# Kernel tuning notes

Hardware: AMD Instinct MI355X
Metric: run time of the kernel (lower is better)

## Reference

```python
import jax, jax.numpy as jnp
import numpy as np

RADIUS = 9.0
GROUPS = 4
BLK = 64  # row block for streaming the N x N pairwise convolution


def leaky(x):
    return jnp.where(x >= 0, x, 0.2 * x)


def group_norm(x, gamma, beta, eps=1e-5):
    # x: (N, C); matches torch.nn.GroupNorm(GROUPS, C) applied to (1, C, N)
    N, C = x.shape
    xg = x.T.reshape(GROUPS, (C // GROUPS) * N)
    m = xg.mean(axis=1, keepdims=True)
    v = ((xg - m) ** 2).mean(axis=1, keepdims=True)
    xg = (xg - m) / jnp.sqrt(v + eps)
    return xg.reshape(C, N).T * gamma + beta


def tangent_vectors(n):
    # Duff et al. orthonormal tangent basis; n: (N,3) unit normals -> (N,2,3)
    x, y, z = n[:, 0], n[:, 1], n[:, 2]
    s = jnp.where(z >= 0, 1.0, -1.0)
    a = -1.0 / (s + z)
    b = x * y * a
    uv = jnp.stack([1 + s * x * x * a, s * b, -s * x, b, s + y * y * a, -y], axis=-1)
    return uv.reshape(-1, 2, 3)


def load_mesh(xyz, normals, weights):
    # Build oriented local frames nuv (N,3,3) as in dMaSIFConv_seg.load_mesh
    p = xyz / RADIUS
    uv = tangent_vectors(normals)                  # (N,2,3)
    diff = p[None, :, :] - p[:, None, :]           # (N,N,3): x_j - x_i
    d2 = jnp.sum(diff * diff, axis=-1)             # (N,N)
    cos = normals @ normals.T                      # (N,N)
    window = jnp.exp(-d2 * (2.0 - cos) ** 2)       # pseudo-geodesic Gaussian
    X = jnp.einsum('ikd,ijd->ijk', uv, diff)       # (N,N,2) tangent coords
    ov = jnp.einsum('ij,j,ijk->ik', window, weights[:, 0], X) + 1e-5  # (N,2)
    nrm = jnp.maximum(jnp.linalg.norm(ov, axis=-1, keepdims=True), 1e-12)
    ov = ov / nrm                                  # F.normalize
    ex, ey = ov[:, :1], ov[:, 1:]
    u, v = uv[:, 0, :], uv[:, 1, :]
    return jnp.stack([normals, ex * u + ey * v, -ey * u + ex * v], axis=1)


def dmasif_conv(points, nuv, feats,
                ni_w1, ni_b1, ni_w2, ni_b2, gn_in_g, gn_in_b,
                cv_a1, cv_b1, cv_a2, cv_b2,
                no_w1, no_b1, no_w2, no_b2, gn_out_g, gn_out_b):
    N = points.shape[0]
    H = ni_w1.shape[0]
    O = no_w1.shape[0]
    # net_in + GroupNorm
    h = leaky(feats @ ni_w1.T + ni_b1)
    h = leaky(h @ ni_w2.T + ni_b2)
    h = group_norm(h, gn_in_g, gn_in_b)            # (N,H)
    p = points / (np.sqrt(2.0) * RADIUS)
    n = jax.lax.stop_gradient(nuv[:, 0, :])        # normals detached in window

    p_blk = p.reshape(-1, BLK, 3)
    n_blk = n.reshape(-1, BLK, 3)
    nuv_blk = nuv.reshape(-1, BLK, 3, 3)

    @jax.checkpoint
    def step(carry, blk):
        pi, ni, nuvi = blk                                  # (B,3),(B,3),(B,3,3)
        diff = p[None, :, :] - pi[:, None, :]               # (B,N,3)
        d2 = jnp.sum(diff * diff, axis=-1)                  # (B,N)
        window = jnp.exp(-d2 * (2.0 - ni @ n.T) ** 2)       # (B,N)
        X = jnp.einsum('bkd,bnd->bnk', nuvi, diff)          # (B,N,3) local coords
        g = jax.nn.relu(jnp.einsum('bnk,ck->bnc', X, cv_a1) + cv_b1)  # (B,N,8)
        M = jax.nn.relu(jnp.einsum('bnc,fc->bnf', g, cv_a2) + cv_b2)  # (B,N,H*O)
        M = M.reshape(BLK, N, O, H)
        out = jnp.einsum('bn,bnoh,nh->bo', window, M, h)    # (B,O)
        return carry, out

    _, outs = jax.lax.scan(step, None, (p_blk, n_blk, nuv_blk))
    y = outs.reshape(N, O)
    y = leaky(y @ no_w1.T + no_b1)
    y = leaky(y @ no_w2.T + no_b2)
    return group_norm(y, gn_out_g, gn_out_b)


def setup_inputs() -> dict:
    key = jax.random.key(0)
    ks = jax.random.split(key, 32)
    N, I, U, H, O, C = 4096, 16, 16, 16, 16, 8
    nrm = jax.random.normal(ks[1], (N, 3), dtype=jnp.float32)
    nrm = nrm / jnp.linalg.norm(nrm, axis=-1, keepdims=True)
    w = lambda k, sh: 0.1 * jax.random.normal(k, sh, dtype=jnp.float32)
    return {
        'surface_xyz': 10.0 * jax.random.normal(ks[0], (N, 3), dtype=jnp.float32),
        'surface_normals': nrm,
        'features': jax.random.normal(ks[2], (N, I), dtype=jnp.float32),
        'os_w1': w(ks[3], (U, I)), 'os_b1': w(ks[4], (U,)),
        'os_w2': w(ks[5], (1, U)), 'os_b2': w(ks[6], (1,)),
        'ni_w1': w(ks[7], (H, I)), 'ni_b1': w(ks[8], (H,)),
        'ni_w2': w(ks[9], (H, H)), 'ni_b2': w(ks[10], (H,)),
        'gn_in_g': jnp.ones((H,), jnp.float32), 'gn_in_b': jnp.zeros((H,), jnp.float32),
        'cv_a1': w(ks[11], (C, 3)), 'cv_b1': w(ks[12], (C,)),
        'cv_a2': w(ks[13], (H * O, C)), 'cv_b2': w(ks[14], (H * O,)),
        'no_w1': w(ks[15], (O, H)), 'no_b1': w(ks[16], (O,)),
        'no_w2': w(ks[17], (O, O)), 'no_b2': w(ks[18], (O,)),
        'gn_out_g': jnp.ones((O,), jnp.float32), 'gn_out_b': jnp.zeros((O,), jnp.float32),
        'll_w1': w(ks[19], (O, O)), 'll_b1': w(ks[20], (O,)),
        'll_w2': w(ks[21], (O, O)), 'll_b2': w(ks[22], (O,)),
        'lt_w': w(ks[23], (O, I)), 'lt_b': w(ks[24], (O,)),
    }


def reference(surface_xyz, surface_normals, features,
              os_w1, os_b1, os_w2, os_b2,
              ni_w1, ni_b1, ni_w2, ni_b2, gn_in_g, gn_in_b,
              cv_a1, cv_b1, cv_a2, cv_b2,
              no_w1, no_b1, no_w2, no_b2, gn_out_g, gn_out_b,
              ll_w1, ll_b1, ll_w2, ll_b2, lt_w, lt_b):
    # orientation scores: Linear -> LeakyReLU(0.2) -> Linear
    scores = leaky(features @ os_w1.T + os_b1) @ os_w2.T + os_b2  # (N,1)
    nuv = load_mesh(surface_xyz, surface_normals, scores)
    # dMaSIFConv_seg forward, n_layers = 1
    x_i = dmasif_conv(surface_xyz, nuv, features,
                      ni_w1, ni_b1, ni_w2, ni_b2, gn_in_g, gn_in_b,
                      cv_a1, cv_b1, cv_a2, cv_b2,
                      no_w1, no_b1, no_w2, no_b2, gn_out_g, gn_out_b)
    x_i = jax.nn.relu(x_i @ ll_w1.T + ll_b1) @ ll_w2.T + ll_b2  # linear_layers[0]
    x = features @ lt_w.T + lt_b                                 # linear_transform[0]
    return x + x_i
```

## Files before the change

kernel.cpp:

```cpp
#include <hip/hip_runtime.h>

#define NP 4096
#define NJC 32
#define JCH (NP / NJC)
#define HR  12

typedef const float* fp;

using half4  = __attribute__((ext_vector_type(4))) __fp16;
using fp16x2 = __attribute__((ext_vector_type(2))) __fp16;
using f32x4  = __attribute__((ext_vector_type(4))) float;

__device__ __forceinline__ float lk(float x) { return x >= 0.f ? x : 0.2f * x; }

__device__ __forceinline__ unsigned int pkrtz(float a, float b) {
    fp16x2 h = __builtin_amdgcn_cvt_pkrtz(a, b);
    unsigned int u; __builtin_memcpy(&u, &h, 4); return u;
}
__device__ __forceinline__ fp16x2 u2h(unsigned int u) {
    fp16x2 h; __builtin_memcpy(&h, &u, 4); return h;
}
__device__ __forceinline__ fp16x2 pkmax0(fp16x2 a, fp16x2 z) {
    fp16x2 d;
    asm("v_pk_max_f16 %0, %1, %2" : "=v"(d) : "v"(a), "v"(z));
    return d;
}

#define OFF_ACC   0
#define OFF_OV    16
#define OFF_CONV  (16 + 2*NP)
#define ZERO_FLTS (16 + 2*NP + 16*NP)
#define OFF_SC    ZERO_FLTS
#define OFF_UV    (OFF_SC  + NP)
#define OFF_P9    (OFF_UV  + 6*NP)
#define OFF_NRM   (OFF_P9  + 3*NP)
#define OFF_HPRE  (OFF_NRM + 3*NP)
#define OFF_HNRM  (OFF_HPRE+ 16*NP)
#define OFF_NUV   (OFF_HNRM+ 16*NP)
#define OFF_Y2    (OFF_NUV + 9*NP)
#define WS_FLTS   (OFF_Y2  + 16*NP)

__global__ __launch_bounds__(256) void k_prep(
    fp xyz, fp nrm, fp feats,
    fp osw1, fp osb1, fp osw2, fp osb2,
    fp niw1, fp nib1, fp niw2, fp nib2,
    float* __restrict__ ws)
{
    const int i = blockIdx.x * 256 + threadIdx.x;

    float f[16];
#pragma unroll
    for (int c = 0; c < 16; c++) f[c] = feats[i * 16 + c];

    float sc = osb2[0];
#pragma unroll
    for (int u = 0; u < 16; u++) {
        float a = osb1[u];
#pragma unroll
        for (int c = 0; c < 16; c++) a += osw1[u * 16 + c] * f[c];
        sc += osw2[u] * lk(a);
    }
    ws[OFF_SC + i] = sc;

    float h1[16];
#pragma unroll
    for (int u = 0; u < 16; u++) {
        float a = nib1[u];
#pragma unroll
        for (int c = 0; c < 16; c++) a += niw1[u * 16 + c] * f[c];
        h1[u] = lk(a);
    }
    float h2[16];
#pragma unroll
    for (int u = 0; u < 16; u++) {
        float a = nib2[u];
#pragma unroll
        for (int c = 0; c < 16; c++) a += niw2[u * 16 + c] * h1[c];
        h2[u] = lk(a);
        ws[OFF_HPRE + i * 16 + u] = h2[u];
    }

#pragma unroll
    for (int g = 0; g < 4; g++) {
        float s = 0.f, ss = 0.f;
#pragma unroll
        for (int k = 0; k < 4; k++) { float v = h2[g * 4 + k]; s += v; ss += v * v; }
#pragma unroll
        for (int off = 32; off > 0; off >>= 1) {
            s  += __shfl_down(s,  off);
            ss += __shfl_down(ss, off);
        }
        if ((threadIdx.x & 63) == 0) {
            atomicAdd(&ws[OFF_ACC + g],     s);
            atomicAdd(&ws[OFF_ACC + 4 + g], ss);
        }
    }

    float nx = nrm[i * 3], ny = nrm[i * 3 + 1], nz = nrm[i * 3 + 2];
    float s  = (nz >= 0.f) ? 1.f : -1.f;
    float a  = -1.f / (s + nz);
    float b  = nx * ny * a;
    float ux = 1.f + s * nx * nx * a, uy = s * b,            uz = -s * nx;
    float vx = b,                     vy = s + ny * ny * a,  vz = -ny;
    ws[OFF_UV + i * 6 + 0] = ux; ws[OFF_UV + i * 6 + 1] = uy; ws[OFF_UV + i * 6 + 2] = uz;
    ws[OFF_UV + i * 6 + 3] = vx; ws[OFF_UV + i * 6 + 4] = vy; ws[OFF_UV + i * 6 + 5] = vz;
    const float IR = 1.f / 9.f;
    ws[OFF_P9 + i * 3 + 0] = xyz[i * 3 + 0] * IR;
    ws[OFF_P9 + i * 3 + 1] = xyz[i * 3 + 1] * IR;
    ws[OFF_P9 + i * 3 + 2] = xyz[i * 3 + 2] * IR;
    ws[OFF_NRM + i * 3 + 0] = nx;
    ws[OFF_NRM + i * 3 + 1] = ny;
    ws[OFF_NRM + i * 3 + 2] = nz;
}

__global__ __launch_bounds__(256) void k_mesh(float* __restrict__ ws)
{
    __shared__ float sp[3][512];
    __shared__ float sn[3][512];
    __shared__ float ssc[512];
    __shared__ float red[256][2];

    const int tid = threadIdx.x;
    const int ib = blockIdx.x >> 3, jc = blockIdx.x & 7;
    const int il = tid & 63, sub = tid >> 6;
    const int i = ib * 64 + il;
    const int j0 = jc * 512;

    for (int t = tid; t < 512; t += 256) {
        int j = j0 + t;
        sp[0][t] = ws[OFF_P9 + j * 3];     sp[1][t] = ws[OFF_P9 + j * 3 + 1];  sp[2][t] = ws[OFF_P9 + j * 3 + 2];
        sn[0][t] = ws[OFF_NRM + j * 3];    sn[1][t] = ws[OFF_NRM + j * 3 + 1]; sn[2][t] = ws[OFF_NRM + j * 3 + 2];
        ssc[t]   = ws[OFF_SC + j];
    }
    __syncthreads();

    const float pix = ws[OFF_P9 + i * 3], piy = ws[OFF_P9 + i * 3 + 1], piz = ws[OFF_P9 + i * 3 + 2];
    const float nix = ws[OFF_NRM + i * 3], niy = ws[OFF_NRM + i * 3 + 1], niz = ws[OFF_NRM + i * 3 + 2];
    const float ux = ws[OFF_UV + i * 6],     uy = ws[OFF_UV + i * 6 + 1], uz = ws[OFF_UV + i * 6 + 2];
    const float vx = ws[OFF_UV + i * 6 + 3], vy = ws[OFF_UV + i * 6 + 4], vz = ws[OFF_UV + i * 6 + 5];

    float ov0 = 0.f, ov1 = 0.f;
#pragma unroll 4
    for (int t = 0; t < 128; t++) {
        int j = sub * 128 + t;
        float dx = sp[0][j] - pix, dy = sp[1][j] - piy, dz = sp[2][j] - piz;
        float d2 = dx * dx + dy * dy + dz * dz;
        float cs = nix * sn[0][j] + niy * sn[1][j] + niz * sn[2][j];
        float tt = 2.f - cs;
        float w  = __expf(-d2 * tt * tt) * ssc[j];
        ov0 += w * (ux * dx + uy * dy + uz * dz);
        ov1 += w * (vx * dx + vy * dy + vz * dz);
    }
    red[tid][0] = ov0; red[tid][1] = ov1;
    __syncthreads();
    if (sub == 0) {
        float a = ov0 + red[64 + il][0] + red[128 + il][0] + red[192 + il][0];
        float b = ov1 + red[64 + il][1] + red[128 + il][1] + red[192 + il][1];
        atomicAdd(&ws[OFF_OV + i * 2],     a);
        atomicAdd(&ws[OFF_OV + i * 2 + 1], b);
    }
}

__global__ __launch_bounds__(256) void k_fin(float* __restrict__ ws, fp gng, fp gnb)
{
    const int i = blockIdx.x * 256 + threadIdx.x;

    float o0 = ws[OFF_OV + i * 2]     + 1e-5f;
    float o1 = ws[OFF_OV + i * 2 + 1] + 1e-5f;
    float nr = fmaxf(sqrtf(o0 * o0 + o1 * o1), 1e-12f);
    float ex = o0 / nr, ey = o1 / nr;

    const float ux = ws[OFF_UV + i * 6],     uy = ws[OFF_UV + i * 6 + 1], uz = ws[OFF_UV + i * 6 + 2];
    const float vx = ws[OFF_UV + i * 6 + 3], vy = ws[OFF_UV + i * 6 + 4], vz = ws[OFF_UV + i * 6 + 5];
    const float nx = ws[OFF_NRM + i * 3], ny = ws[OFF_NRM + i * 3 + 1], nz = ws[OFF_NRM + i * 3 + 2];

    ws[OFF_NUV + i * 9 + 0] = nx;
    ws[OFF_NUV + i * 9 + 1] = ny;
    ws[OFF_NUV + i * 9 + 2] = nz;
    ws[OFF_NUV + i * 9 + 3] =  ex * ux + ey * vx;
    ws[OFF_NUV + i * 9 + 4] =  ex * uy + ey * vy;
    ws[OFF_NUV + i * 9 + 5] =  ex * uz + ey * vz;
    ws[OFF_NUV + i * 9 + 6] = -ey * ux + ex * vx;
    ws[OFF_NUV + i * 9 + 7] = -ey * uy + ex * vy;
    ws[OFF_NUV + i * 9 + 8] = -ey * uz + ex * vz;

    const float invM = 1.f / (4.f * NP);
#pragma unroll
    for (int c = 0; c < 16; c++) {
        int g = c >> 2;
        float m   = ws[OFF_ACC + g] * invM;
        float var = ws[OFF_ACC + 4 + g] * invM - m * m;
        float inv = rsqrtf(var + 1e-5f);
        ws[OFF_HNRM + i * 16 + c] =
            (ws[OFF_HPRE + i * 16 + c] - m) * inv * gng[c] + gnb[c];
    }
}

__global__ __launch_bounds__(256, 4) void k_conv(
    const float* __restrict__ ws,
    const float* __restrict__ cva1, const float* __restrict__ cvb1,
    const float* __restrict__ A2,   const float* __restrict__ B2,
    float* __restrict__ conv)
{
    __shared__ float4 sP[JCH];
    __shared__ float4 sN[JCH];
    __shared__ __align__(16) unsigned int sH2[JCH * HR];

    const int tid  = threadIdx.x;
    const int ib   = blockIdx.x >> 5;
    const int jc   = blockIdx.x & 31;
    const int j0   = jc * JCH;
    const int lane = tid & 63;
    const int wv   = tid >> 6;
    const int o    = lane & 15;
    const int quad = lane >> 4;
    const float IVS2 = 0.70710678118654752f;

    if (tid < JCH) {
        const int t = tid;
        const int j = j0 + t;
        sP[t] = make_float4(ws[OFF_P9 + j * 3] * IVS2,
                            ws[OFF_P9 + j * 3 + 1] * IVS2,
                            ws[OFF_P9 + j * 3 + 2] * IVS2, 0.f);
        sN[t] = make_float4(ws[OFF_NRM + j * 3],
                            ws[OFF_NRM + j * 3 + 1],
                            ws[OFF_NRM + j * 3 + 2], 0.f);
        const float4* hs = (const float4*)(ws + OFF_HNRM + j * 16);
        float4 h0 = hs[0], h1 = hs[1], h2 = hs[2], h3 = hs[3];
        uint4 w0, w1;
        w0.x = pkrtz(h0.x, h0.y); w0.y = pkrtz(h0.z, h0.w);
        w0.z = pkrtz(h1.x, h1.y); w0.w = pkrtz(h1.z, h1.w);
        w1.x = pkrtz(h2.x, h2.y); w1.y = pkrtz(h2.z, h2.w);
        w1.z = pkrtz(h3.x, h3.y); w1.w = pkrtz(h3.z, h3.w);
        *(uint4*)(sH2 + t * HR)     = w0;
        *(uint4*)(sH2 + t * HR + 4) = w1;
    }

    half4 Bf[16];
#pragma unroll
    for (int t = 0; t < 16; t++) {
        half4 v = {(__fp16)0.f, (__fp16)0.f, (__fp16)0.f, (__fp16)0.f};
        const float* row = A2 + (o * 16 + t) * 8;
        if (quad == 0) {
#pragma unroll
            for (int c = 0; c < 4; c++) v[c] = (__fp16)row[c];
        } else if (quad == 1) {
#pragma unroll
            for (int c = 0; c < 4; c++) v[c] = (__fp16)row[4 + c];
        } else if (quad == 2) {
            v[0] = (__fp16)B2[o * 16 + t];
        }
        Bf[t] = v;
    }

    float a1[24], b1c[8];
#pragma unroll
    for (int k = 0; k < 24; k++) a1[k] = cva1[k];
#pragma unroll
    for (int k = 0; k < 8; k++)  b1c[k] = cvb1[k];

    __syncthreads();

    const f32x4 zc = {0.f, 0.f, 0.f, 0.f};
    const fp16x2 h2z = {(__fp16)0.f, (__fp16)0.f};
    const int o4 = o << 2;

#pragma unroll 1
    for (int ii = 0; ii < 16; ii++) {
        const int i = ib * 64 + wv * 16 + ii;
        const float pix = ws[OFF_P9 + i * 3 + 0] * IVS2;
        const float piy = ws[OFF_P9 + i * 3 + 1] * IVS2;
        const float piz = ws[OFF_P9 + i * 3 + 2] * IVS2;
        float r[9];
#pragma unroll
        for (int k = 0; k < 9; k++) r[k] = ws[OFF_NUV + i * 9 + k];

        float accO = 0.f;

#pragma unroll 1
        for (int jg = 0; jg < JCH / 64; jg++) {
            const int jl = jg * 64 + lane;
            const float4 pj = sP[jl];
            const float4 nj = sN[jl];
            const float dx = pj.x - pix, dy = pj.y - piy, dz = pj.z - piz;
            const float d2 = dx * dx + dy * dy + dz * dz;
            const float cs = r[0] * nj.x + r[1] * nj.y + r[2] * nj.z;
            const float tt = 2.f - cs;
            const float wwin = __expf(-d2 * tt * tt);
            const float X0 = r[0] * dx + r[1] * dy + r[2] * dz;
            const float X1 = r[3] * dx + r[4] * dy + r[5] * dz;
            const float X2 = r[6] * dx + r[7] * dy + r[8] * dz;
            float g[8];
#pragma unroll
            for (int c = 0; c < 8; c++)
                g[c] = fmaxf(a1[c * 3] * X0 + a1[c * 3 + 1] * X1 +
                             a1[c * 3 + 2] * X2 + b1c[c], 0.f);
            const int wg0 = (int)pkrtz(wwin * g[0], wwin * g[1]);
            const int wg1 = (int)pkrtz(wwin * g[2], wwin * g[3]);
            const int wg2 = (int)pkrtz(wwin * g[4], wwin * g[5]);
            const int wg3 = (int)pkrtz(wwin * g[6], wwin * g[7]);
            const int whp = (int)pkrtz(wwin, 0.f);

#pragma unroll 1
            for (int tau = 0; tau < 4; tau++) {
                const int srcb = tau * 64 + o4;
                const unsigned u0 = (unsigned)__builtin_amdgcn_ds_bpermute(srcb, wg0);
                const unsigned u1 = (unsigned)__builtin_amdgcn_ds_bpermute(srcb, wg1);
                const unsigned u2 = (unsigned)__builtin_amdgcn_ds_bpermute(srcb, wg2);
                const unsigned u3 = (unsigned)__builtin_amdgcn_ds_bpermute(srcb, wg3);
                const unsigned uw = (unsigned)__builtin_amdgcn_ds_bpermute(srcb, whp);
                uint2 av;
                av.x = (quad == 0) ? u0 : (quad == 1) ? u2 : (quad == 2) ? uw : 0u;
                av.y = (quad == 0) ? u1 : (quad == 1) ? u3 : 0u;
                half4 Af; __builtin_memcpy(&Af, &av, 8);

#pragma unroll
                for (int hq = 0; hq < 2; hq++) {
                    fp16x2 P[16];
#pragma unroll
                    for (int q2 = 0; q2 < 4; q2++) {
                        const int q = hq * 4 + q2;
                        f32x4 C0 = __builtin_amdgcn_mfma_f32_16x16x16f16(Af, Bf[2 * q],     zc, 0, 0, 0);
                        f32x4 C1 = __builtin_amdgcn_mfma_f32_16x16x16f16(Af, Bf[2 * q + 1], zc, 0, 0, 0);
#pragma unroll
                        for (int r2 = 0; r2 < 4; r2++) {
                            fp16x2 pp = __builtin_amdgcn_cvt_pkrtz(C0[r2], C1[r2]);
                            P[r2 * 4 + q2] = pkmax0(pp, h2z);
                        }
                    }
#pragma unroll
                    for (int r2 = 0; r2 < 4; r2++) {
                        const unsigned int* hr =
                            sH2 + (jg * 64 + tau * 16 + quad * 4 + r2) * HR + hq * 4;
                        const uint4 ha = *(const uint4*)hr;
                        accO = __builtin_amdgcn_fdot2(P[r2 * 4 + 0], u2h(ha.x), accO, false);
                        accO = __builtin_amdgcn_fdot2(P[r2 * 4 + 1], u2h(ha.y), accO, false);
                        accO = __builtin_amdgcn_fdot2(P[r2 * 4 + 2], u2h(ha.z), accO, false);
                        accO = __builtin_amdgcn_fdot2(P[r2 * 4 + 3], u2h(ha.w), accO, false);
                    }
                }
            }
        }

        accO += __shfl_xor(accO, 16, 64);
        accO += __shfl_xor(accO, 32, 64);
        if (lane < 16) atomicAdd(&conv[i * 16 + o], accO);
    }
}

__global__ __launch_bounds__(256) void k_post1(
    float* __restrict__ ws, fp now1, fp nob1, fp now2, fp nob2)
{
    const int i = blockIdx.x * 256 + threadIdx.x;
    float cv[16];
#pragma unroll
    for (int o = 0; o < 16; o++) cv[o] = ws[OFF_CONV + i * 16 + o];

    float y1[16];
#pragma unroll
    for (int u = 0; u < 16; u++) {
        float a = nob1[u];
#pragma unroll
        for (int k = 0; k < 16; k++) a += now1[u * 16 + k] * cv[k];
        y1[u] = lk(a);
    }
    float y2[16];
#pragma unroll
    for (int u = 0; u < 16; u++) {
        float a = nob2[u];
#pragma unroll
        for (int k = 0; k < 16; k++) a += now2[u * 16 + k] * y1[k];
        y2[u] = lk(a);
        ws[OFF_Y2 + i * 16 + u] = y2[u];
    }
#pragma unroll
    for (int g = 0; g < 4; g++) {
        float s = 0.f, ss = 0.f;
#pragma unroll
        for (int k = 0; k < 4; k++) { float v = y2[g * 4 + k]; s += v; ss += v * v; }
#pragma unroll
        for (int off = 32; off > 0; off >>= 1) {
            s  += __shfl_down(s,  off);
            ss += __shfl_down(ss, off);
        }
        if ((threadIdx.x & 63) == 0) {
            atomicAdd(&ws[OFF_ACC + 8 + g],  s);
            atomicAdd(&ws[OFF_ACC + 12 + g], ss);
        }
    }
}

__global__ __launch_bounds__(256) void k_post2(
    const float* __restrict__ ws, fp feats, fp gg, fp gb,
    fp llw1, fp llb1, fp llw2, fp llb2, fp ltw, fp ltb,
    float* __restrict__ out)
{
    const int i = blockIdx.x * 256 + threadIdx.x;
    const float invM = 1.f / (4.f * NP);

    float z[16];
#pragma unroll
    for (int c = 0; c < 16; c++) {
        int g = c >> 2;
        float m   = ws[OFF_ACC + 8 + g] * invM;
        float var = ws[OFF_ACC + 12 + g] * invM - m * m;
        float inv = rsqrtf(var + 1e-5f);
        z[c] = (ws[OFF_Y2 + i * 16 + c] - m) * inv * gg[c] + gb[c];
    }
    float r1[16];
#pragma unroll
    for (int o = 0; o < 16; o++) {
        float a = llb1[o];
#pragma unroll
        for (int k = 0; k < 16; k++) a += llw1[o * 16 + k] * z[k];
        r1[o] = fmaxf(a, 0.f);
    }
    float f[16];
#pragma unroll
    for (int c = 0; c < 16; c++) f[c] = feats[i * 16 + c];
#pragma unroll
    for (int o = 0; o < 16; o++) {
        float a = llb2[o];
#pragma unroll
        for (int k = 0; k < 16; k++) a += llw2[o * 16 + k] * r1[k];
        float x = ltb[o];
#pragma unroll
        for (int k = 0; k < 16; k++) x += ltw[o * 16 + k] * f[k];
        out[i * 16 + o] = x + a;
    }
}

extern "C" void kernel_launch(void* const* d_in, const int* in_sizes, int n_in,
                              void* d_out, int out_size, void* d_ws, size_t ws_size,
                              hipStream_t stream)
{
    fp xyz  = (fp)d_in[0];
    fp nrm  = (fp)d_in[1];
    fp fts  = (fp)d_in[2];
    fp osw1 = (fp)d_in[3],  osb1 = (fp)d_in[4],  osw2 = (fp)d_in[5],  osb2 = (fp)d_in[6];
    fp niw1 = (fp)d_in[7],  nib1 = (fp)d_in[8],  niw2 = (fp)d_in[9],  nib2 = (fp)d_in[10];
    fp gng  = (fp)d_in[11], gnb  = (fp)d_in[12];
    fp cva1 = (fp)d_in[13], cvb1 = (fp)d_in[14], cva2 = (fp)d_in[15], cvb2 = (fp)d_in[16];
    fp now1 = (fp)d_in[17], nob1 = (fp)d_in[18], now2 = (fp)d_in[19], nob2 = (fp)d_in[20];
    fp gog  = (fp)d_in[21], gob  = (fp)d_in[22];
    fp llw1 = (fp)d_in[23], llb1 = (fp)d_in[24], llw2 = (fp)d_in[25], llb2 = (fp)d_in[26];
    fp ltw  = (fp)d_in[27], ltb  = (fp)d_in[28];

    float* ws = (float*)d_ws;

    (void)hipMemsetAsync(d_ws, 0, (size_t)ZERO_FLTS * sizeof(float), stream);
    k_prep<<<NP / 256, 256, 0, stream>>>(xyz, nrm, fts,
                                         osw1, osb1, osw2, osb2,
                                         niw1, nib1, niw2, nib2, ws);
    k_mesh<<<512, 256, 0, stream>>>(ws);
    k_fin<<<NP / 256, 256, 0, stream>>>(ws, gng, gnb);
    k_conv<<<64 * NJC, 256, 0, stream>>>(ws, cva1, cvb1, cva2, cvb2, ws + OFF_CONV);
    k_post1<<<NP / 256, 256, 0, stream>>>(ws, now1, nob1, now2, nob2);
    k_post2<<<NP / 256, 256, 0, stream>>>(ws, fts, gog, gob,
                                          llw1, llb1, llw2, llb2, ltw, ltb,
                                          (float*)d_out);
}
```

Before: 472.9 us.

## Fuse finalize and post kernels, drop memset, use grid-wide counter for GroupNorm stats

Removes the memset by zeroing accumulators inside k_prep. Folds k_fin into k_conv: the GroupNorm of the hidden features and the local-frame construction are now recomputed per block from per-block partial sums. k_post1 and k_post2 become one kernel that shares GroupNorm statistics through a spin-wait grid barrier on an atomic counter. This cuts three launches and the round trips of intermediate buffers. The cost is redundant per-block recomputation, and the barrier relies on all 16 blocks being co-resident.

```diff
diff --git a/kernel.cpp b/kernel.cpp
--- a/kernel.cpp
+++ b/kernel.cpp
@@ -26,19 +26,17 @@
     return d;
 }
 
-#define OFF_ACC   0
-#define OFF_OV    16
-#define OFF_CONV  (16 + 2*NP)
-#define ZERO_FLTS (16 + 2*NP + 16*NP)
-#define OFF_SC    ZERO_FLTS
+#define OFF_CTR   0
+#define OFF_PART1 4
+#define OFF_PART2 132
+#define OFF_OV    260
+#define OFF_CONV  (260 + 2*NP)
+#define OFF_SC    (260 + 18*NP)
 #define OFF_UV    (OFF_SC  + NP)
 #define OFF_P9    (OFF_UV  + 6*NP)
 #define OFF_NRM   (OFF_P9  + 3*NP)
 #define OFF_HPRE  (OFF_NRM + 3*NP)
-#define OFF_HNRM  (OFF_HPRE+ 16*NP)
-#define OFF_NUV   (OFF_HNRM+ 16*NP)
-#define OFF_Y2    (OFF_NUV + 9*NP)
-#define WS_FLTS   (OFF_Y2  + 16*NP)
+#define WS_FLTS   (OFF_HPRE+ 16*NP)
 
 __global__ __launch_bounds__(256) void k_prep(
     fp xyz, fp nrm, fp feats,
@@ -46,7 +44,19 @@
     fp niw1, fp nib1, fp niw2, fp nib2,
     float* __restrict__ ws)
 {
-    const int i = blockIdx.x * 256 + threadIdx.x;
+    __shared__ float sR[4][8];
+    const int tid = threadIdx.x;
+    const int i = blockIdx.x * 256 + tid;
+    const int wv = tid >> 6;
+
+    ws[OFF_OV + i * 2]     = 0.f;
+    ws[OFF_OV + i * 2 + 1] = 0.f;
+    {
+        float4 z4 = make_float4(0.f, 0.f, 0.f, 0.f);
+        float4* c4 = (float4*)(ws + OFF_CONV + i * 16);
+        c4[0] = z4; c4[1] = z4; c4[2] = z4; c4[3] = z4;
+    }
+    if (blockIdx.x == 0 && tid == 0) *(unsigned*)(ws + OFF_CTR) = 0u;
 
     float f[16];
 #pragma unroll
@@ -90,10 +100,12 @@
             s  += __shfl_down(s,  off);
             ss += __shfl_down(ss, off);
         }
-        if ((threadIdx.x & 63) == 0) {
-            atomicAdd(&ws[OFF_ACC + g],     s);
-            atomicAdd(&ws[OFF_ACC + 4 + g], ss);
-        }
+        if ((tid & 63) == 0) { sR[wv][g] = s; sR[wv][4 + g] = ss; }
+    }
+    __syncthreads();
+    if (tid < 8) {
+        float v = sR[0][tid] + sR[1][tid] + sR[2][tid] + sR[3][tid];
+        ws[OFF_PART1 + blockIdx.x * 8 + tid] = v;
     }
 
     float nx = nrm[i * 3], ny = nrm[i * 3 + 1], nz = nrm[i * 3 + 2];
@@ -161,50 +173,17 @@
     }
 }
 
-__global__ __launch_bounds__(256) void k_fin(float* __restrict__ ws, fp gng, fp gnb)
-{
-    const int i = blockIdx.x * 256 + threadIdx.x;
-
-    float o0 = ws[OFF_OV + i * 2]     + 1e-5f;
-    float o1 = ws[OFF_OV + i * 2 + 1] + 1e-5f;
-    float nr = fmaxf(sqrtf(o0 * o0 + o1 * o1), 1e-12f);
-    float ex = o0 / nr, ey = o1 / nr;
-
-    const float ux = ws[OFF_UV + i * 6],     uy = ws[OFF_UV + i * 6 + 1], uz = ws[OFF_UV + i * 6 + 2];
-    const float vx = ws[OFF_UV + i * 6 + 3], vy = ws[OFF_UV + i * 6 + 4], vz = ws[OFF_UV + i * 6 + 5];
-    const float nx = ws[OFF_NRM + i * 3], ny = ws[OFF_NRM + i * 3 + 1], nz = ws[OFF_NRM + i * 3 + 2];
-
-    ws[OFF_NUV + i * 9 + 0] = nx;
-    ws[OFF_NUV + i * 9 + 1] = ny;
-    ws[OFF_NUV + i * 9 + 2] = nz;
-    ws[OFF_NUV + i * 9 + 3] =  ex * ux + ey * vx;
-    ws[OFF_NUV + i * 9 + 4] =  ex * uy + ey * vy;
-    ws[OFF_NUV + i * 9 + 5] =  ex * uz + ey * vz;
-    ws[OFF_NUV + i * 9 + 6] = -ey * ux + ex * vx;
-    ws[OFF_NUV + i * 9 + 7] = -ey * uy + ex * vy;
-    ws[OFF_NUV + i * 9 + 8] = -ey * uz + ex * vz;
-
-    const float invM = 1.f / (4.f * NP);
-#pragma unroll
-    for (int c = 0; c < 16; c++) {
-        int g = c >> 2;
-        float m   = ws[OFF_ACC + g] * invM;
-        float var = ws[OFF_ACC + 4 + g] * invM - m * m;
-        float inv = rsqrtf(var + 1e-5f);
-        ws[OFF_HNRM + i * 16 + c] =
-            (ws[OFF_HPRE + i * 16 + c] - m) * inv * gng[c] + gnb[c];
-    }
-}
-
 __global__ __launch_bounds__(256, 4) void k_conv(
     const float* __restrict__ ws,
     const float* __restrict__ cva1, const float* __restrict__ cvb1,
     const float* __restrict__ A2,   const float* __restrict__ B2,
+    fp gng, fp gnb,
     float* __restrict__ conv)
 {
     __shared__ float4 sP[JCH];
     __shared__ float4 sN[JCH];
     __shared__ __align__(16) unsigned int sH2[JCH * HR];
+    __shared__ float sGN[8];
 
     const int tid  = threadIdx.x;
     const int ib   = blockIdx.x >> 5;
@@ -216,6 +195,21 @@
     const int quad = lane >> 4;
     const float IVS2 = 0.70710678118654752f;
 
+    if (tid < 4) {
+        float s = 0.f, q = 0.f;
+#pragma unroll
+        for (int b = 0; b < 16; b++) {
+            s += ws[OFF_PART1 + b * 8 + tid];
+            q += ws[OFF_PART1 + b * 8 + 4 + tid];
+        }
+        const float invM = 1.f / (4.f * NP);
+        float m   = s * invM;
+        float var = q * invM - m * m;
+        sGN[tid]     = m;
+        sGN[4 + tid] = rsqrtf(var + 1e-5f);
+    }
+    __syncthreads();
+
     if (tid < JCH) {
         const int t = tid;
         const int j = j0 + t;
@@ -225,8 +219,22 @@
         sN[t] = make_float4(ws[OFF_NRM + j * 3],
                             ws[OFF_NRM + j * 3 + 1],
                             ws[OFF_NRM + j * 3 + 2], 0.f);
-        const float4* hs = (const float4*)(ws + OFF_HNRM + j * 16);
+        const float4* hs = (const float4*)(ws + OFF_HPRE + j * 16);
         float4 h0 = hs[0], h1 = hs[1], h2 = hs[2], h3 = hs[3];
+        const float4* gg4 = (const float4*)gng;
+        const float4* gb4 = (const float4*)gnb;
+        float4 ga0 = gg4[0], ga1 = gg4[1], ga2 = gg4[2], ga3 = gg4[3];
+        float4 gb0 = gb4[0], gb1 = gb4[1], gb2 = gb4[2], gb3 = gb4[3];
+        const float m0 = sGN[0], m1 = sGN[1], m2 = sGN[2], m3 = sGN[3];
+        const float v0 = sGN[4], v1 = sGN[5], v2 = sGN[6], v3 = sGN[7];
+        h0.x = (h0.x - m0) * v0 * ga0.x + gb0.x; h0.y = (h0.y - m0) * v0 * ga0.y + gb0.y;
+        h0.z = (h0.z - m0) * v0 * ga0.z + gb0.z; h0.w = (h0.w - m0) * v0 * ga0.w + gb0.w;
+        h1.x = (h1.x - m1) * v1 * ga1.x + gb1.x; h1.y = (h1.y - m1) * v1 * ga1.y + gb1.y;
+        h1.z = (h1.z - m1) * v1 * ga1.z + gb1.z; h1.w = (h1.w - m1) * v1 * ga1.w + gb1.w;
+        h2.x = (h2.x - m2) * v2 * ga2.x + gb2.x; h2.y = (h2.y - m2) * v2 * ga2.y + gb2.y;
+        h2.z = (h2.z - m2) * v2 * ga2.z + gb2.z; h2.w = (h2.w - m2) * v2 * ga2.w + gb2.w;
+        h3.x = (h3.x - m3) * v3 * ga3.x + gb3.x; h3.y = (h3.y - m3) * v3 * ga3.y + gb3.y;
+        h3.z = (h3.z - m3) * v3 * ga3.z + gb3.z; h3.w = (h3.w - m3) * v3 * ga3.w + gb3.w;
         uint4 w0, w1;
         w0.x = pkrtz(h0.x, h0.y); w0.y = pkrtz(h0.z, h0.w);
         w0.z = pkrtz(h1.x, h1.y); w0.w = pkrtz(h1.z, h1.w);
@@ -272,8 +280,23 @@
         const float piy = ws[OFF_P9 + i * 3 + 1] * IVS2;
         const float piz = ws[OFF_P9 + i * 3 + 2] * IVS2;
         float r[9];
-#pragma unroll
-        for (int k = 0; k < 9; k++) r[k] = ws[OFF_NUV + i * 9 + k];
+        {
+            float o0 = ws[OFF_OV + i * 2]     + 1e-5f;
+            float o1 = ws[OFF_OV + i * 2 + 1] + 1e-5f;
+            float nr = fmaxf(sqrtf(o0 * o0 + o1 * o1), 1e-12f);
+            float ex = o0 / nr, ey = o1 / nr;
+            float ux = ws[OFF_UV + i * 6],     uy = ws[OFF_UV + i * 6 + 1], uz = ws[OFF_UV + i * 6 + 2];
+            float vx = ws[OFF_UV + i * 6 + 3], vy = ws[OFF_UV + i * 6 + 4], vz = ws[OFF_UV + i * 6 + 5];
+            r[0] = ws[OFF_NRM + i * 3];
+            r[1] = ws[OFF_NRM + i * 3 + 1];
+            r[2] = ws[OFF_NRM + i * 3 + 2];
+            r[3] =  ex * ux + ey * vx;
+            r[4] =  ex * uy + ey * vy;
+            r[5] =  ex * uz + ey * vz;
+            r[6] = -ey * ux + ex * vx;
+            r[7] = -ey * uy + ex * vy;
+            r[8] = -ey * uz + ex * vz;
+        }
 
         float accO = 0.f;
 
@@ -348,10 +371,19 @@
     }
 }
 
-__global__ __launch_bounds__(256) void k_post1(
-    float* __restrict__ ws, fp now1, fp nob1, fp now2, fp nob2)
+__global__ __launch_bounds__(256) void k_post(
+    float* __restrict__ ws, fp feats,
+    fp now1, fp nob1, fp now2, fp nob2,
+    fp gg, fp gb,
+    fp llw1, fp llb1, fp llw2, fp llb2, fp ltw, fp ltb,
+    float* __restrict__ out)
 {
-    const int i = blockIdx.x * 256 + threadIdx.x;
+    __shared__ float sR[4][8];
+    __shared__ float sP2[128];
+    const int tid = threadIdx.x;
+    const int i = blockIdx.x * 256 + tid;
+    const int wv = tid >> 6;
+
     float cv[16];
 #pragma unroll
     for (int o = 0; o < 16; o++) cv[o] = ws[OFF_CONV + i * 16 + o];
@@ -371,8 +403,8 @@
 #pragma unroll
         for (int k = 0; k < 16; k++) a += now2[u * 16 + k] * y1[k];
         y2[u] = lk(a);
-        ws[OFF_Y2 + i * 16 + u] = y2[u];
-    }
+    }
+
 #pragma unroll
     for (int g = 0; g < 4; g++) {
         float s = 0.f, ss = 0.f;
@@ -383,29 +415,41 @@
             s  += __shfl_down(s,  off);
             ss += __shfl_down(ss, off);
         }
-        if ((threadIdx.x & 63) == 0) {
-            atomicAdd(&ws[OFF_ACC + 8 + g],  s);
-            atomicAdd(&ws[OFF_ACC + 12 + g], ss);
-        }
-    }
-}
-
-__global__ __launch_bounds__(256) void k_post2(
-    const float* __restrict__ ws, fp feats, fp gg, fp gb,
-    fp llw1, fp llb1, fp llw2, fp llb2, fp ltw, fp ltb,
-    float* __restrict__ out)
-{
-    const int i = blockIdx.x * 256 + threadIdx.x;
+        if ((tid & 63) == 0) { sR[wv][g] = s; sR[wv][4 + g] = ss; }
+    }
+    __syncthreads();
+    if (tid < 8) {
+        float v = sR[0][tid] + sR[1][tid] + sR[2][tid] + sR[3][tid];
+        __hip_atomic_store(&ws[OFF_PART2 + blockIdx.x * 8 + tid], v,
+                           __ATOMIC_RELEASE, __HIP_MEMORY_SCOPE_AGENT);
+    }
+    __syncthreads();
+
+    unsigned* ctr = (unsigned*)(ws + OFF_CTR);
+    if (tid == 0) {
+        __hip_atomic_fetch_add(ctr, 1u, __ATOMIC_ACQ_REL, __HIP_MEMORY_SCOPE_AGENT);
+        while (__hip_atomic_load(ctr, __ATOMIC_ACQUIRE, __HIP_MEMORY_SCOPE_AGENT) < gridDim.x)
+            __builtin_amdgcn_s_sleep(8);
+    }
+    __syncthreads();
+
+    if (tid < 128)
+        sP2[tid] = __hip_atomic_load(&ws[OFF_PART2 + tid],
+                                     __ATOMIC_ACQUIRE, __HIP_MEMORY_SCOPE_AGENT);
+    __syncthreads();
+
     const float invM = 1.f / (4.f * NP);
-
     float z[16];
 #pragma unroll
     for (int c = 0; c < 16; c++) {
         int g = c >> 2;
-        float m   = ws[OFF_ACC + 8 + g] * invM;
-        float var = ws[OFF_ACC + 12 + g] * invM - m * m;
+        float s = 0.f, q = 0.f;
+#pragma unroll
+        for (int b = 0; b < 16; b++) { s += sP2[b * 8 + g]; q += sP2[b * 8 + 4 + g]; }
+        float m   = s * invM;
+        float var = q * invM - m * m;
         float inv = rsqrtf(var + 1e-5f);
-        z[c] = (ws[OFF_Y2 + i * 16 + c] - m) * inv * gg[c] + gb[c];
+        z[c] = (y2[c] - m) * inv * gg[c] + gb[c];
     }
     float r1[16];
 #pragma unroll
@@ -448,15 +492,13 @@
 
     float* ws = (float*)d_ws;
 
-    (void)hipMemsetAsync(d_ws, 0, (size_t)ZERO_FLTS * sizeof(float), stream);
     k_prep<<<NP / 256, 256, 0, stream>>>(xyz, nrm, fts,
                                          osw1, osb1, osw2, osb2,
                                          niw1, nib1, niw2, nib2, ws);
     k_mesh<<<512, 256, 0, stream>>>(ws);
-    k_fin<<<NP / 256, 256, 0, stream>>>(ws, gng, gnb);
-    k_conv<<<64 * NJC, 256, 0, stream>>>(ws, cva1, cvb1, cva2, cvb2, ws + OFF_CONV);
-    k_post1<<<NP / 256, 256, 0, stream>>>(ws, now1, nob1, now2, nob2);
-    k_post2<<<NP / 256, 256, 0, stream>>>(ws, fts, gog, gob,
-                                          llw1, llb1, llw2, llb2, ltw, ltb,
-                                          (float*)d_out);
-}
+    k_conv<<<64 * NJC, 256, 0, stream>>>(ws, cva1, cvb1, cva2, cvb2,
+                                         gng, gnb, ws + OFF_CONV);
+    k_post<<<NP / 256, 256, 0, stream>>>(ws, fts, now1, nob1, now2, nob2,
+                                         gog, gob, llw1, llb1, llw2, llb2,
+                                         ltw, ltb, (float*)d_out);
+}
```

Measured after the change: 471.4 us. No clear change (-0.3%).
